# Kernel optimization log

Measured on AMD Instinct MI355X. Metric: run time of the kernel, lower is better.

Reference implementation:

```python
import jax, jax.numpy as jnp
import numpy as np

B, L, F = 256, 512, 64
NUM_IDS = 2000
LN_EPS = 1e-5


def setup_inputs() -> dict:
    key = jax.random.key(0)
    ks = jax.random.split(key, 16)
    s = 0.05
    return {
        # padded neighbor-id sequences; 0 is the padding id
        "src_ids": jax.random.randint(ks[0], (B, L), 0, NUM_IDS, dtype=jnp.int64)
        if jax.config.jax_enable_x64 else jax.random.randint(ks[0], (B, L), 0, NUM_IDS, dtype=jnp.int32),
        "dst_ids": jax.random.randint(ks[1], (B, L), 0, NUM_IDS, dtype=jnp.int64)
        if jax.config.jax_enable_x64 else jax.random.randint(ks[1], (B, L), 0, NUM_IDS, dtype=jnp.int32),
        # co-occurrence encode MLP: Linear(1->F), ReLU, Linear(F->F)
        "enc_w1": jax.random.normal(ks[2], (1, F), jnp.float32) * s,
        "enc_b1": jax.random.normal(ks[3], (F,), jnp.float32) * s,
        "enc_w2": jax.random.normal(ks[4], (F, F), jnp.float32) * s,
        "enc_b2": jax.random.normal(ks[5], (F,), jnp.float32) * s,
        # cross-attention projections (bias-free q/k/v as in source)
        "Wq": jax.random.normal(ks[6], (F, F), jnp.float32) * s,
        "Wk": jax.random.normal(ks[7], (F, F), jnp.float32) * s,
        "Wv": jax.random.normal(ks[8], (F, F), jnp.float32) * s,
        "Wo": jax.random.normal(ks[9], (F, F), jnp.float32) * s,
        "bo": jax.random.normal(ks[10], (F,), jnp.float32) * s,
        "ln_g": jnp.ones((F,), jnp.float32),
        "ln_b": jnp.zeros((F,), jnp.float32),
    }


def _counts_in(a, b):
    # for each element of a: how many times does it occur in b (same batch row)
    # equivalent to the np.unique count / mapping-dict lookup in the original
    return (a[:, :, None] == b[:, None, :]).sum(axis=-1).astype(jnp.float32)


def _appearances(a, b):
    # [B, L, 2]: counts of each id of `a` in (a, b); zero out padding (id==0)
    app = jnp.stack([_counts_in(a, a), _counts_in(a, b)], axis=-1)
    return jnp.where((a == 0)[..., None], 0.0, app)


def _encode(app, w1, b1, w2, b2):
    # Linear(1->F) -> ReLU -> Linear(F->F), then sum over the 2 count channels
    h = jax.nn.relu(app[..., None] * w1[0] + b1)  # [B, L, 2, F]
    h = jnp.einsum('blcf,fg->blcg', h, w2) + b2
    return h.sum(axis=2)  # [B, L, F]


def _linear_attn(q, k, v):
    dim = q.shape[-1]
    q = jax.nn.softmax(q, axis=-1) * (dim ** -0.5)
    k = jax.nn.softmax(k, axis=1)  # softmax over sequence dim (dim=-2)
    ctx = jnp.einsum('bld,ble->bde', k, v)
    return jnp.einsum('bld,bde->ble', q, ctx)


def _layer_norm(x, g, b):
    mu = x.mean(axis=-1, keepdims=True)
    var = ((x - mu) ** 2).mean(axis=-1, keepdims=True)
    return (x - mu) * jax.lax.rsqrt(var + LN_EPS) * g + b


def _cross_attn(x, ctx, Wq, Wk, Wv, Wo, bo, ln_g, ln_b):
    q, k, v = x @ Wq, ctx @ Wk, ctx @ Wv
    attn = _linear_attn(q, k, v)
    return _layer_norm(x + attn @ Wo + bo, ln_g, ln_b)


def reference(src_ids, dst_ids, enc_w1, enc_b1, enc_w2, enc_b2,
              Wq, Wk, Wv, Wo, bo, ln_g, ln_b):
    # neighbor co-occurrence counting + encoding
    src_app = _appearances(src_ids, dst_ids)  # [B, L, 2]
    dst_app = _appearances(dst_ids, src_ids)
    src_feat = _encode(src_app, enc_w1, enc_b1, enc_w2, enc_b2)  # [B, L, F]
    dst_feat = _encode(dst_app, enc_w1, enc_b1, enc_w2, enc_b2)
    # linear cross-attention fusion (shared weights, both directions)
    src_out = _cross_attn(src_feat, dst_feat, Wq, Wk, Wv, Wo, bo, ln_g, ln_b)
    dst_out = _cross_attn(dst_feat, src_feat, Wq, Wk, Wv, Wo, bo, ln_g, ln_b)
    return jnp.stack([src_out, dst_out])  # [2, B, L, F]
```

## Files before the change

kernel.cpp:

```cpp
#include <hip/hip_runtime.h>

#define BB 256
#define LL 512

typedef float nfloat4 __attribute__((ext_vector_type(4)));

__global__ __launch_bounds__(256, 2) void k_all(
    const int* __restrict__ src, const int* __restrict__ dst,
    const float* __restrict__ w1, const float* __restrict__ b1,
    const float* __restrict__ w2, const float* __restrict__ b2,
    const float* __restrict__ Wq, const float* __restrict__ Wk,
    const float* __restrict__ Wv, const float* __restrict__ Wo,
    const float* __restrict__ bo, const float* __restrict__ lng,
    const float* __restrict__ lnb, float* __restrict__ out) {
  __shared__ __align__(16) char smem[63776];
  int*   hist  = (int*)smem;
  float* poolF = (float*)smem;
  int*   hkey  = (int*)(smem + 16384);
  int*   hmult = (int*)(smem + 20480);
  float* tabL  = (float*)(smem + 16384);
  float* Mg    = (float*)(smem + 32768);
  int*   xkey  = (int*)(smem + 50176);
  int*   ckey  = (int*)(smem + 52224);
  int*   cmult = (int*)(smem + 54272);
  int*   pidxl = (int*)(smem + 56320);
  int*   cflag = (int*)(smem + 58368);
  int*   clist = (int*)(smem + 60424);
  float* fbF   = (float*)(smem + 60688);
  int*   npp   = (int*)(smem + 63760);

  int bd = blockIdx.x, b = bd >> 1, dir = bd & 1;
  int tid = threadIdx.x, tx = tid & 63, ty = tid >> 6;
  int e0 = ty * 16;

  const int* s = src + b * LL;
  const int* d = dst + b * LL;
  int sid0 = s[tid], sid1 = s[tid + 256];
  int did0 = d[tid], did1 = d[tid + 256];

  float wcA[64], wcB[64];
#pragma unroll
  for (int f = 0; f < 64; ++f) wcA[f] = w2[f * 64 + tx];
  float w1v = w1[tx], b1v = b1[tx], b2v = b2[tx];

  for (int i = tid; i < 2000; i += 256) hist[i] = 0;
  for (int i = tid; i < 1024; i += 256) { hkey[i] = -1; hmult[i] = 0; }
  for (int i = tid; i < 513; i += 256) cflag[i] = 0;
  if (tid < 3) npp[tid] = 0;
  __syncthreads();

  atomicAdd(&hist[sid0], 1);      atomicAdd(&hist[sid1], 1);
  atomicAdd(&hist[did0], 65536);  atomicAdd(&hist[did1], 65536);
  __syncthreads();

  int x0 = dir ? did0 : sid0, x1 = dir ? did1 : sid1;
  int c0 = dir ? sid0 : did0, c1 = dir ? sid1 : did1;

  int slot0 = 0, slot1 = 0;
#pragma unroll
  for (int r = 0; r < 4; ++r) {
    int side = r >> 1;
    int id = (r == 0) ? c0 : (r == 1) ? c1 : (r == 2) ? x0 : x1;
    int ca = 0, cb = 0;
    if (id != 0) {
      int hv = hist[id];
      int cs = hv & 0xffff, cd2 = hv >> 16;
      if (side != dir) { ca = cs; cb = cd2; }
      else             { ca = cd2; cb = cs; }
    }
    int key = ca | (cb << 10) | (side << 20);
    int h = (int)(((unsigned)key * 2654435761u) >> 22) & 1023;
    while (true) {
      int old = atomicCAS(&hkey[h], -1, key);
      if (old == -1 || old == key) break;
      h = (h + 1) & 1023;
    }
    if (side == 0) atomicAdd(&hmult[h], 1);
    else if (r == 2) slot0 = h;
    else slot1 = h;
  }
  __syncthreads();

  for (int i = tid; i < 1024; i += 256) {
    int k = hkey[i];
    if (k != -1) {
      if (k & (1 << 20)) {
        int idx = atomicAdd(&npp[1], 1);
        xkey[idx] = k & 0xFFFFF;
        hkey[i] = idx;
      } else {
        int idx = atomicAdd(&npp[0], 1);
        ckey[idx]  = k;
        cmult[idx] = hmult[i];
      }
    }
  }
  __syncthreads();
  int Pc = npp[0], Px = npp[1];
  pidxl[tid]       = hkey[slot0];
  pidxl[tid + 256] = hkey[slot1];
  for (int i = tid; i < Pc; i += 256) { int k = ckey[i]; cflag[k & 1023] = 1; cflag[k >> 10] = 1; }
  for (int i = tid; i < Px; i += 256) { int k = xkey[i]; cflag[k & 1023] = 1; cflag[k >> 10] = 1; }
  __syncthreads();
  for (int c = tid; c < 513; c += 256) {
    if (cflag[c]) {
      int idx = atomicAdd(&npp[2], 1);
      clist[idx] = c;
      cflag[c] = idx;
    }
  }
  __syncthreads();
  int nc = npp[2];
  for (int i = tid; i < Pc; i += 256) { int k = ckey[i]; ckey[i] = cflag[k & 1023] | (cflag[k >> 10] << 10); }
  for (int i = tid; i < Px; i += 256) { int k = xkey[i]; xkey[i] = cflag[k & 1023] | (cflag[k >> 10] << 10); }

  for (int i = ty; i < nc; i += 4) {
    float c = (float)clist[i];
    fbF[ty * 64 + tx] = fmaxf(c * w1v + b1v, 0.f);
    float acc = b2v;
    const float4* h4 = (const float4*)&fbF[ty * 64];
#pragma unroll
    for (int q = 0; q < 16; ++q) {
      float4 hv = h4[q];
      acc += hv.x * wcA[4 * q] + hv.y * wcA[4 * q + 1] + hv.z * wcA[4 * q + 2] + hv.w * wcA[4 * q + 3];
    }
    tabL[i * 64 + tx] = acc;
  }
#pragma unroll
  for (int f = 0; f < 64; ++f) { wcA[f] = Wk[f * 64 + tx]; wcB[f] = Wv[f * 64 + tx]; }
  float macc[16];
#pragma unroll
  for (int e = 0; e < 16; ++e) macc[e] = 0.f;
  float sacc = 0.f;
  __syncthreads();

  float* pA = poolF;
  float* vA = poolF + 2048;
  for (int j0 = 0; j0 < Pc; j0 += 32) {
    int cN = min(32, Pc - j0);
    for (int j = ty; j < cN; j += 4) {
      int key = ckey[j0 + j];
      int ia = key & 1023, ib = key >> 10;
      fbF[ty * 64 + tx] = tabL[ia * 64 + tx] + tabL[ib * 64 + tx];
      float kr = 0.f, vr = 0.f;
      const float4* fb4 = (const float4*)&fbF[ty * 64];
#pragma unroll
      for (int q = 0; q < 16; ++q) {
        float4 fv = fb4[q];
        kr += fv.x * wcA[4 * q] + fv.y * wcA[4 * q + 1] + fv.z * wcA[4 * q + 2] + fv.w * wcA[4 * q + 3];
        vr += fv.x * wcB[4 * q] + fv.y * wcB[4 * q + 1] + fv.z * wcB[4 * q + 2] + fv.w * wcB[4 * q + 3];
      }
      float p = __expf(kr) * (float)cmult[j0 + j];
      sacc += p;
      pA[j * 64 + tx] = p;
      vA[j * 64 + tx] = vr;
    }
    if (j0 + 32 >= Pc) fbF[512 + ty * 64 + tx] = sacc;
    __syncthreads();
    for (int jj = 0; jj < cN; ++jj) {
      float pg = pA[jj * 64 + tx];
      const float4* vb4 = (const float4*)&vA[jj * 64 + e0];
#pragma unroll
      for (int q = 0; q < 4; ++q) {
        float4 vv = vb4[q];
        macc[4 * q]     += pg * vv.x; macc[4 * q + 1] += pg * vv.y;
        macc[4 * q + 2] += pg * vv.z; macc[4 * q + 3] += pg * vv.w;
      }
    }
    __syncthreads();
  }
  float inv = 1.f / (fbF[512 + tx] + fbF[576 + tx] + fbF[640 + tx] + fbF[704 + tx]);
#pragma unroll
  for (int e = 0; e < 16; ++e) Mg[(e0 + e) * 68 + tx] = macc[e] * inv;
#pragma unroll
  for (int f = 0; f < 64; ++f) { wcA[f] = Wq[f * 64 + tx]; wcB[f] = Wo[f * 64 + tx]; }
  float bov = bo[tx], lg = lng[tx], lb = lnb[tx];
  __syncthreads();

  for (int i0 = 0; i0 < Px; i0 += 64) {
    int cN = min(64, Px - i0);
    for (int jj = ty; jj < cN; jj += 4) {
      int key = xkey[i0 + jj];
      int ia = key & 1023, ib = key >> 10;
      float fv = tabL[ia * 64 + tx] + tabL[ib * 64 + tx];
      fbF[ty * 64 + tx] = fv;
      float qr = 0.f;
      const float4* fb4 = (const float4*)&fbF[ty * 64];
#pragma unroll
      for (int q = 0; q < 16; ++q) {
        float4 f4v = fb4[q];
        qr += f4v.x * wcA[4 * q] + f4v.y * wcA[4 * q + 1] + f4v.z * wcA[4 * q + 2] + f4v.w * wcA[4 * q + 3];
      }
      float p = __expf(qr);
      float sum = p;
#pragma unroll
      for (int off = 32; off >= 1; off >>= 1) sum += __shfl_xor(sum, off, 64);
      float qh = p / sum * 0.125f;
      fbF[256 + ty * 64 + tx] = qh;
      float t = 0.f;
      const float4* qb4 = (const float4*)&fbF[256 + ty * 64];
      const float4* mt4 = (const float4*)&Mg[tx * 68];
#pragma unroll
      for (int q = 0; q < 16; ++q) {
        float4 qv = qb4[q];
        float4 mv = mt4[q];
        t += qv.x * mv.x + qv.y * mv.y + qv.z * mv.z + qv.w * mv.w;
      }
      fbF[512 + ty * 64 + tx] = t;
      float at = 0.f;
      const float4* tb4 = (const float4*)&fbF[512 + ty * 64];
#pragma unroll
      for (int q = 0; q < 16; ++q) {
        float4 tv = tb4[q];
        at += tv.x * wcB[4 * q] + tv.y * wcB[4 * q + 1] + tv.z * wcB[4 * q + 2] + tv.w * wcB[4 * q + 3];
      }
      float r = fv + at + bov;
      float mu = r;
#pragma unroll
      for (int off = 32; off >= 1; off >>= 1) mu += __shfl_xor(mu, off, 64);
      mu *= (1.f / 64.f);
      float dv = r - mu;
      float var = dv * dv;
#pragma unroll
      for (int off = 32; off >= 1; off >>= 1) var += __shfl_xor(var, off, 64);
      var *= (1.f / 64.f);
      poolF[jj * 64 + tx] = dv * rsqrtf(var + 1e-5f) * lg + lb;
    }
    __syncthreads();
    const nfloat4* w4 = (const nfloat4*)poolF;
    nfloat4* out4 = (nfloat4*)(out + (size_t)(dir * BB + b) * (LL * 64));
    for (int idx = tid; idx < 512 * 16; idx += 256) {
      int l = idx >> 4, q = idx & 15;
      int pid = pidxl[l];
      if (pid >= i0 && pid < i0 + cN)
        __builtin_nontemporal_store(w4[(pid - i0) * 16 + q], &out4[l * 16 + q]);
    }
    __syncthreads();
  }
}

extern "C" void kernel_launch(void* const* d_in, const int* in_sizes, int n_in,
                              void* d_out, int out_size, void* d_ws, size_t ws_size,
                              hipStream_t stream) {
  const int* src  = (const int*)d_in[0];
  const int* dst  = (const int*)d_in[1];
  const float* w1 = (const float*)d_in[2];
  const float* b1 = (const float*)d_in[3];
  const float* w2 = (const float*)d_in[4];
  const float* b2 = (const float*)d_in[5];
  const float* Wq = (const float*)d_in[6];
  const float* Wk = (const float*)d_in[7];
  const float* Wv = (const float*)d_in[8];
  const float* Wo = (const float*)d_in[9];
  const float* bo = (const float*)d_in[10];
  const float* lng = (const float*)d_in[11];
  const float* lnb = (const float*)d_in[12];
  float* out = (float*)d_out;

  k_all<<<dim3(512), dim3(256), 0, stream>>>(src, dst, w1, b1, w2, b2,
                                             Wq, Wk, Wv, Wo, bo, lng, lnb, out);
}
```

Measured before the change: 117.9 us.

## Replace hash-table pattern dedup with direct-mapped table over compacted counts

```diff
diff --git a/kernel.cpp b/kernel.cpp
--- a/kernel.cpp
+++ b/kernel.cpp
@@ -4,6 +4,7 @@
 #define LL 512
 
 typedef float nfloat4 __attribute__((ext_vector_type(4)));
+typedef int   nint4   __attribute__((ext_vector_type(4)));
 
 __global__ __launch_bounds__(256, 2) void k_all(
     const int* __restrict__ src, const int* __restrict__ dst,
@@ -16,9 +17,9 @@
   __shared__ __align__(16) char smem[63776];
   int*   hist  = (int*)smem;
   float* poolF = (float*)smem;
-  int*   hkey  = (int*)(smem + 16384);
-  int*   hmult = (int*)(smem + 20480);
+  int*   dmapc = (int*)(smem + 16384);
   float* tabL  = (float*)(smem + 16384);
+  int*   dmapx = (int*)(smem + 32768);
   float* Mg    = (float*)(smem + 32768);
   int*   xkey  = (int*)(smem + 50176);
   int*   ckey  = (int*)(smem + 52224);
@@ -43,10 +44,17 @@
   for (int f = 0; f < 64; ++f) wcA[f] = w2[f * 64 + tx];
   float w1v = w1[tx], b1v = b1[tx], b2v = b2[tx];
 
-  for (int i = tid; i < 2000; i += 256) hist[i] = 0;
-  for (int i = tid; i < 1024; i += 256) { hkey[i] = -1; hmult[i] = 0; }
-  for (int i = tid; i < 513; i += 256) cflag[i] = 0;
-  if (tid < 3) npp[tid] = 0;
+  {
+    nint4 z4 = {0, 0, 0, 0};
+    nint4* h4z = (nint4*)hist;
+    for (int i = tid; i < 500; i += 256) h4z[i] = z4;
+    nint4* dm4 = (nint4*)dmapc;
+    for (int i = tid; i < 2048; i += 256) dm4[i] = z4;
+    nint4* cf4 = (nint4*)cflag;
+    if (tid < 128) cf4[tid] = z4;
+    if (tid == 0) cflag[512] = 0;
+    if (tid < 3) npp[tid] = 0;
+  }
   __syncthreads();
 
   atomicAdd(&hist[sid0], 1);      atomicAdd(&hist[sid1], 1);
@@ -54,54 +62,14 @@
   __syncthreads();
 
   int x0 = dir ? did0 : sid0, x1 = dir ? did1 : sid1;
-  int c0 = dir ? sid0 : did0, c1 = dir ? sid1 : did1;
-
-  int slot0 = 0, slot1 = 0;
-#pragma unroll
-  for (int r = 0; r < 4; ++r) {
-    int side = r >> 1;
-    int id = (r == 0) ? c0 : (r == 1) ? c1 : (r == 2) ? x0 : x1;
-    int ca = 0, cb = 0;
-    if (id != 0) {
-      int hv = hist[id];
-      int cs = hv & 0xffff, cd2 = hv >> 16;
-      if (side != dir) { ca = cs; cb = cd2; }
-      else             { ca = cd2; cb = cs; }
-    }
-    int key = ca | (cb << 10) | (side << 20);
-    int h = (int)(((unsigned)key * 2654435761u) >> 22) & 1023;
-    while (true) {
-      int old = atomicCAS(&hkey[h], -1, key);
-      if (old == -1 || old == key) break;
-      h = (h + 1) & 1023;
-    }
-    if (side == 0) atomicAdd(&hmult[h], 1);
-    else if (r == 2) slot0 = h;
-    else slot1 = h;
-  }
-  __syncthreads();
-
-  for (int i = tid; i < 1024; i += 256) {
-    int k = hkey[i];
-    if (k != -1) {
-      if (k & (1 << 20)) {
-        int idx = atomicAdd(&npp[1], 1);
-        xkey[idx] = k & 0xFFFFF;
-        hkey[i] = idx;
-      } else {
-        int idx = atomicAdd(&npp[0], 1);
-        ckey[idx]  = k;
-        cmult[idx] = hmult[i];
-      }
-    }
-  }
-  __syncthreads();
-  int Pc = npp[0], Px = npp[1];
-  pidxl[tid]       = hkey[slot0];
-  pidxl[tid + 256] = hkey[slot1];
-  for (int i = tid; i < Pc; i += 256) { int k = ckey[i]; cflag[k & 1023] = 1; cflag[k >> 10] = 1; }
-  for (int i = tid; i < Px; i += 256) { int k = xkey[i]; cflag[k & 1023] = 1; cflag[k >> 10] = 1; }
-  __syncthreads();
+
+  for (int i = tid; i < 2000; i += 256) {
+    int hv = hist[i];
+    if (i != 0 && hv != 0) { cflag[hv & 0xffff] = 1; cflag[hv >> 16] = 1; }
+  }
+  if (tid == 0) cflag[0] = 1;
+  __syncthreads();
+
   for (int c = tid; c < 513; c += 256) {
     if (cflag[c]) {
       int idx = atomicAdd(&npp[2], 1);
@@ -110,10 +78,51 @@
     }
   }
   __syncthreads();
-  int nc = npp[2];
-  for (int i = tid; i < Pc; i += 256) { int k = ckey[i]; ckey[i] = cflag[k & 1023] | (cflag[k >> 10] << 10); }
-  for (int i = tid; i < Px; i += 256) { int k = xkey[i]; xkey[i] = cflag[k & 1023] | (cflag[k >> 10] << 10); }
-
+
+  for (int i = tid; i < 2000; i += 256) {
+    int hv = hist[i];
+    if (i == 0 || hv == 0) continue;
+    int cs = hv & 0xffff, cd = hv >> 16;
+    int k = cflag[min(cs, cd)] * 64 + cflag[max(cs, cd)];
+    int ox = dir ? cd : cs;
+    int oc = dir ? cs : cd;
+    if (ox) dmapx[k] = 1;
+    if (oc) atomicAdd(&dmapc[k], oc);
+  }
+  if (tid == 0) {
+    int hv = hist[0];
+    int cs = hv & 0xffff, cd = hv >> 16;
+    int k00 = cflag[0] * 65;
+    int ox = dir ? cd : cs, oc = dir ? cs : cd;
+    if (ox) dmapx[k00] = 1;
+    if (oc) atomicAdd(&dmapc[k00], oc);
+  }
+  __syncthreads();
+
+  for (int i = tid; i < 4096; i += 256) {
+    int v = dmapc[i];
+    if (v) { int idx = atomicAdd(&npp[0], 1); ckey[idx] = i; cmult[idx] = v; }
+    int xv = dmapx[i];
+    if (xv) { int idx = atomicAdd(&npp[1], 1); xkey[idx] = i; dmapx[i] = idx; }
+  }
+  __syncthreads();
+  int Pc = npp[0], Px = npp[1], nc = npp[2];
+
+  {
+    int hvx0 = (x0 == 0) ? 0 : hist[x0];
+    int hvx1 = (x1 == 0) ? 0 : hist[x1];
+    int k0, k1;
+    {
+      int cs = hvx0 & 0xffff, cd = hvx0 >> 16;
+      k0 = (x0 == 0) ? cflag[0] * 65 : cflag[min(cs, cd)] * 64 + cflag[max(cs, cd)];
+    }
+    {
+      int cs = hvx1 & 0xffff, cd = hvx1 >> 16;
+      k1 = (x1 == 0) ? cflag[0] * 65 : cflag[min(cs, cd)] * 64 + cflag[max(cs, cd)];
+    }
+    pidxl[tid]       = dmapx[k0];
+    pidxl[tid + 256] = dmapx[k1];
+  }
   for (int i = ty; i < nc; i += 4) {
     float c = (float)clist[i];
     fbF[ty * 64 + tx] = fmaxf(c * w1v + b1v, 0.f);
@@ -140,7 +149,7 @@
     int cN = min(32, Pc - j0);
     for (int j = ty; j < cN; j += 4) {
       int key = ckey[j0 + j];
-      int ia = key & 1023, ib = key >> 10;
+      int ia = key >> 6, ib = key & 63;
       fbF[ty * 64 + tx] = tabL[ia * 64 + tx] + tabL[ib * 64 + tx];
       float kr = 0.f, vr = 0.f;
       const float4* fb4 = (const float4*)&fbF[ty * 64];
@@ -181,7 +190,7 @@
     int cN = min(64, Px - i0);
     for (int jj = ty; jj < cN; jj += 4) {
       int key = xkey[i0 + jj];
-      int ia = key & 1023, ib = key >> 10;
+      int ia = key >> 6, ib = key & 63;
       float fv = tabL[ia * 64 + tx] + tabL[ib * 64 + tx];
       fbF[ty * 64 + tx] = fv;
       float qr = 0.f;
```

After: 118.7 us. Within noise of the previous version (+0.7%).
